# Kernel optimization log

Hardware: AMD Instinct MI355X
Metric: run time of the kernel (lower is better)

The kernel has to match this reference:

```python
import jax, jax.numpy as jnp
import numpy as np

NG, ND, NS, E, DIM, H = 20000, 8000, 8000, 300000, 256, 8
HD = DIM // H
SCALE = 1.0 / float(np.sqrt(HD))
EPS = 1e-5


def _ln(x, g, b):
    mu = x.mean(-1, keepdims=True)
    var = ((x - mu) ** 2).mean(-1, keepdims=True)
    return (x - mu) / jnp.sqrt(var + EPS) * g + b


def _attn(h_src, h_dst, Wq, bq, Wk, bk, Wv, bv, src, dst, n_dst):
    # multi-head edge dot-product attention with edge_softmax over incoming edges
    Q = (h_dst @ Wq.T + bq).reshape(-1, H, HD)
    K = (h_src @ Wk.T + bk).reshape(-1, H, HD)
    V = (h_src @ Wv.T + bv).reshape(-1, H, HD)
    score = jnp.einsum('ehd,ehd->eh', K[src], Q[dst]) * SCALE  # [E, H]
    m = jax.ops.segment_max(score, dst, num_segments=n_dst)
    m = jnp.where(jnp.isfinite(m), m, 0.0)  # nodes with no in-edges
    a = jnp.exp(score - m[dst])
    denom = jax.ops.segment_sum(a, dst, num_segments=n_dst)
    a = a / denom[dst]
    h = jax.ops.segment_sum(V[src] * a[:, :, None], dst, num_segments=n_dst)
    return h.reshape(n_dst, DIM)


def _bahdanau(m1, m2, W1, b1, W2, b2, v, bv):
    e1 = (jnp.tanh(m1 @ W1.T + b1) @ v.T + bv)[:, 0]
    e2 = (jnp.tanh(m2 @ W2.T + b2) @ v.T + bv)[:, 0]
    w = jax.nn.softmax(jnp.stack([e1, e2], axis=1), axis=1)
    return w[:, 0:1] * m1 + w[:, 1:2] * m2


def _forward(gene_feat, drug_feat, disease_feat,
             dg_Wq, dg_bq, dg_Wk, dg_bk, dg_Wv, dg_bv,
             disg_Wq, disg_bq, disg_Wk, disg_bk, disg_Wv, disg_bv,
             gd_Wq, gd_bq, gd_Wk, gd_bk, gd_Wv, gd_bv,
             gdis_Wq, gdis_bq, gdis_Wk, gdis_bk, gdis_Wv, gdis_bv,
             f_W1, f_b1, f_W2, f_b2, f_v, f_bv,
             ln1_g, ln1_b, ln2_g, ln2_b,
             dg_src, dg_dst, disg_src, disg_dst, gd_src, gd_dst, gdis_src, gdis_dst):
    gm_drug = _attn(drug_feat, gene_feat, dg_Wq, dg_bq, dg_Wk, dg_bk, dg_Wv, dg_bv, dg_src, dg_dst, NG)
    gm_dis = _attn(disease_feat, gene_feat, disg_Wq, disg_bq, disg_Wk, disg_bk, disg_Wv, disg_bv, disg_src, disg_dst, NG)
    has_d = jnp.zeros((NG,), bool).at[dg_dst].set(True)
    has_s = jnp.zeros((NG,), bool).at[disg_dst].set(True)
    fused = _bahdanau(gm_drug, gm_dis, f_W1, f_b1, f_W2, f_b2, f_v, f_bv)
    gene_msg = jnp.where((has_d & has_s)[:, None], fused,
                         jnp.where(has_d[:, None], gm_drug,
                                   jnp.where(has_s[:, None], gm_dis, 0.0)))
    gene_out = _ln(gene_feat + jax.nn.gelu(gene_msg, approximate=False), ln1_g, ln1_b)
    drug_msg = _attn(gene_out, drug_feat, gd_Wq, gd_bq, gd_Wk, gd_bk, gd_Wv, gd_bv, gd_src, gd_dst, ND)
    dis_msg = _attn(gene_out, disease_feat, gdis_Wq, gdis_bq, gdis_Wk, gdis_bk, gdis_Wv, gdis_bv, gdis_src, gdis_dst, NS)
    drug_out = _ln(drug_feat + jax.nn.gelu(drug_msg, approximate=False), ln2_g, ln2_b)
    disease_out = _ln(disease_feat + jax.nn.gelu(dis_msg, approximate=False), ln2_g, ln2_b)
    return (drug_out, disease_out, gene_out)


def setup_inputs() -> dict:
    ks = jax.random.split(jax.random.key(0), 40)
    it = iter(range(40))

    def nrm(shape):
        return jax.random.normal(ks[next(it)], shape, dtype=jnp.float32)

    def xav(din, dout):
        lim = float(np.sqrt(6.0 / (din + dout)))
        return jax.random.uniform(ks[next(it)], (dout, din), minval=-lim, maxval=lim, dtype=jnp.float32)

    def ridx(n, hi):
        return jax.random.randint(ks[next(it)], (n,), 0, hi, dtype=jnp.int32)

    inp = {}
    inp['gene_feat'] = nrm((NG, DIM))
    inp['drug_feat'] = nrm((ND, DIM))
    inp['disease_feat'] = nrm((NS, DIM))
    for p in ['dg', 'disg', 'gd', 'gdis']:
        inp[p + '_Wq'] = xav(DIM, DIM)
        inp[p + '_bq'] = jnp.zeros((DIM,), jnp.float32)
        inp[p + '_Wk'] = xav(DIM, DIM)
        inp[p + '_bk'] = jnp.zeros((DIM,), jnp.float32)
        inp[p + '_Wv'] = xav(DIM, DIM)
        inp[p + '_bv'] = jnp.zeros((DIM,), jnp.float32)
    inp['f_W1'] = xav(DIM, DIM); inp['f_b1'] = jnp.zeros((DIM,), jnp.float32)
    inp['f_W2'] = xav(DIM, DIM); inp['f_b2'] = jnp.zeros((DIM,), jnp.float32)
    inp['f_v'] = xav(DIM, 1); inp['f_bv'] = jnp.zeros((1,), jnp.float32)
    inp['ln1_g'] = jnp.ones((DIM,), jnp.float32); inp['ln1_b'] = jnp.zeros((DIM,), jnp.float32)
    inp['ln2_g'] = jnp.ones((DIM,), jnp.float32); inp['ln2_b'] = jnp.zeros((DIM,), jnp.float32)
    inp['dg_src'] = ridx(E, ND); inp['dg_dst'] = ridx(E, NG)
    inp['disg_src'] = ridx(E, NS); inp['disg_dst'] = ridx(E, NG)
    inp['gd_src'] = ridx(E, NG); inp['gd_dst'] = ridx(E, ND)
    inp['gdis_src'] = ridx(E, NG); inp['gdis_dst'] = ridx(E, NS)
    return inp


def reference(gene_feat, drug_feat, disease_feat,
              dg_Wq, dg_bq, dg_Wk, dg_bk, dg_Wv, dg_bv,
              disg_Wq, disg_bq, disg_Wk, disg_bk, disg_Wv, disg_bv,
              gd_Wq, gd_bq, gd_Wk, gd_bk, gd_Wv, gd_bv,
              gdis_Wq, gdis_bq, gdis_Wk, gdis_bk, gdis_Wv, gdis_bv,
              f_W1, f_b1, f_W2, f_b2, f_v, f_bv,
              ln1_g, ln1_b, ln2_g, ln2_b,
              dg_src, dg_dst, disg_src, disg_dst, gd_src, gd_dst, gdis_src, gdis_dst):
    return _forward(gene_feat, drug_feat, disease_feat,
                    dg_Wq, dg_bq, dg_Wk, dg_bk, dg_Wv, dg_bv,
                    disg_Wq, disg_bq, disg_Wk, disg_bk, disg_Wv, disg_bv,
                    gd_Wq, gd_bq, gd_Wk, gd_bk, gd_Wv, gd_bv,
                    gdis_Wq, gdis_bq, gdis_Wk, gdis_bk, gdis_Wv, gdis_bv,
                    f_W1, f_b1, f_W2, f_b2, f_v, f_bv,
                    ln1_g, ln1_b, ln2_g, ln2_b,
                    dg_src, dg_dst, disg_src, disg_dst, gd_src, gd_dst, gdis_src, gdis_dst)
```

## Files before the change

### kernel.cpp

```cpp
#include <hip/hip_runtime.h>

#define NG 20000
#define ND 8000
#define NS 8000
#define EE 300000
#define DIM 256
#define SCALE_QK 0.17677669529663687f
#define LNEPS 1e-5f

#define MAXB 40
#define L1CH 2048
#define NCH1 ((EE + L1CH - 1) / L1CH)
#define CB_G 8704
#define CB_S 10496
#define RB_G (40 * CB_G)
#define RB_S (32 * CB_S)

typedef __attribute__((ext_vector_type(4))) float floatx4;
typedef __attribute__((ext_vector_type(8))) short shortx8;
typedef __attribute__((ext_vector_type(8))) unsigned short ushortx8;

__device__ __forceinline__ float bf2f(unsigned short u) {
    union { unsigned u; float f; } c; c.u = ((unsigned)u) << 16; return c.f;
}
__device__ __forceinline__ unsigned short f2bf(float f) {
    union { float f; unsigned u; } c; c.f = f;
    return (unsigned short)((c.u + 0x7fffu + ((c.u >> 16) & 1u)) >> 16);
}
__device__ __forceinline__ float gelu_exact(float v) {
    return 0.5f * v * (1.0f + erff(v * 0.70710678118654752f));
}

template <int MODE, int KVI>
__global__ __launch_bounds__(256, 2) void gemm_nt(
    const unsigned short* __restrict__ A, const unsigned short* __restrict__ W,
    const float* __restrict__ bias1, const float* __restrict__ bias2,
    const float* __restrict__ bias3, const float* __restrict__ bias4,
    unsigned short* __restrict__ C, int ldc,
    const float* __restrict__ vvec, float* __restrict__ evec, int M)
{
    __shared__ unsigned short As[128][40];
    __shared__ unsigned short Bs[64][40];
    const int tid = threadIdx.x;
    const int lane = tid & 63, wv = tid >> 6;
    const int quad = lane >> 4, l16 = lane & 15;
    const int m0 = blockIdx.x * 128;
    const int n0 = blockIdx.y * 64;

    floatx4 acc[2][4];
#pragma unroll
    for (int i = 0; i < 2; ++i)
#pragma unroll
        for (int j = 0; j < 4; ++j) acc[i][j] = (floatx4){0.f, 0.f, 0.f, 0.f};

    const int sr = tid >> 2;
    const int sc = (tid & 3) * 8;

    for (int k0 = 0; k0 < 256; k0 += 32) {
        __syncthreads();
        *(int4*)(&Bs[sr][sc]) =
            *(const int4*)(W + (size_t)(n0 + sr) * 256 + k0 + sc);
#pragma unroll
        for (int rr = 0; rr < 2; ++rr) {
            int row = sr + rr * 64;
            int gm = m0 + row;
            int4 av = make_int4(0, 0, 0, 0);
            if (gm < M)
                av = *(const int4*)(A + (size_t)gm * 256 + k0 + sc);
            *(int4*)(&As[row][sc]) = av;
        }
        __syncthreads();
        shortx8 af[2], bfr[4];
#pragma unroll
        for (int mf = 0; mf < 2; ++mf)
            af[mf] = *(const shortx8*)(&As[wv * 32 + mf * 16 + l16][quad * 8]);
#pragma unroll
        for (int nf = 0; nf < 4; ++nf)
            bfr[nf] = *(const shortx8*)(&Bs[nf * 16 + l16][quad * 8]);
#pragma unroll
        for (int mf = 0; mf < 2; ++mf)
#pragma unroll
            for (int nf = 0; nf < 4; ++nf)
                acc[mf][nf] = __builtin_amdgcn_mfma_f32_16x16x32_bf16(
                    af[mf], bfr[nf], acc[mf][nf], 0, 0, 0);
    }

    if (MODE == 0) {
#pragma unroll
        for (int mf = 0; mf < 2; ++mf)
#pragma unroll
            for (int r = 0; r < 4; ++r) {
                int m = m0 + wv * 32 + mf * 16 + quad * 4 + r;
                if (m < M) {
#pragma unroll
                    for (int nf = 0; nf < 4; ++nf) {
                        int n = n0 + nf * 16 + l16;
                        int h = n >> 8;
                        const float* bp = (h == 0) ? bias1 : (h == 1) ? bias2
                                        : (h == 2) ? bias3 : bias4;
                        float bn = bp[n & 255];
                        int pos;
                        if (KVI) {
                            int nn = n & 511;
                            pos = (n & ~511) + ((nn & 255) >> 2) * 8 + (nn & 3) +
                                  ((nn >> 8) << 2);
                        } else {
                            pos = n;
                        }
                        C[(size_t)m * ldc + pos] = f2bf(acc[mf][nf][r] + bn);
                    }
                }
            }
    } else {
        float p[2][4] = {};
#pragma unroll
        for (int mf = 0; mf < 2; ++mf)
#pragma unroll
            for (int nf = 0; nf < 4; ++nf) {
                int n = n0 + nf * 16 + l16;
                float vn = vvec[n];
                float bn = bias1[n];
#pragma unroll
                for (int r = 0; r < 4; ++r)
                    p[mf][r] += vn * tanhf(acc[mf][nf][r] + bn);
            }
#pragma unroll
        for (int mf = 0; mf < 2; ++mf)
#pragma unroll
            for (int r = 0; r < 4; ++r) {
                float s = p[mf][r];
                s += __shfl_xor(s, 1); s += __shfl_xor(s, 2);
                s += __shfl_xor(s, 4); s += __shfl_xor(s, 8);
                if (l16 == 0) {
                    int m = m0 + wv * 32 + mf * 16 + quad * 4 + r;
                    if (m < M) atomicAdd(&evec[m], s);
                }
            }
    }
}

struct WSrc { const float* p[14]; };

__global__ void convert_w_kernel(WSrc s, unsigned short* __restrict__ out) {
    int idx = blockIdx.x * 256 + threadIdx.x;
    int mat = idx >> 14;
    int e = (idx & 16383) << 2;
    float4 f = *(const float4*)(s.p[mat] + e);
    ushort4 t;
    t.x = f2bf(f.x); t.y = f2bf(f.y); t.z = f2bf(f.z); t.w = f2bf(f.w);
    *(ushort4*)(out + ((size_t)mat << 16) + e) = t;
}

__global__ void convert_feat_kernel(
    const float* __restrict__ gf, const float* __restrict__ df,
    const float* __restrict__ sf, unsigned short* __restrict__ go,
    unsigned short* __restrict__ dougo, unsigned short* __restrict__ so)
{
    const int NG4 = NG * 64, ND4 = ND * 64, NS4 = NS * 64;
    int i = blockIdx.x * 256 + threadIdx.x;
    const float* in; unsigned short* out; int j;
    if (i < NG4) { in = gf; out = go; j = i; }
    else if (i < NG4 + ND4) { in = df; out = dougo; j = i - NG4; }
    else if (i < NG4 + ND4 + NS4) { in = sf; out = so; j = i - NG4 - ND4; }
    else return;
    float4 f = *(const float4*)(in + (size_t)j * 4);
    ushort4 t;
    t.x = f2bf(f.x); t.y = f2bf(f.y); t.z = f2bf(f.z); t.w = f2bf(f.w);
    *(ushort4*)(out + (size_t)j * 4) = t;
}

__global__ void zero_kernel(int* __restrict__ p, int n) {
    int i = blockIdx.x * blockDim.x + threadIdx.x;
    if (i < n) p[i] = 0;
}
__global__ void fillf_kernel(float* __restrict__ p, int n, float v) {
    int i = blockIdx.x * blockDim.x + threadIdx.x;
    if (i < n) p[i] = v;
}

struct L1P {
    const int* src[4];
    const int* dst[4];
    int* brec[4];
    int* bcur;
};
__global__ __launch_bounds__(256) void l1_bucket_kernel(L1P a) {
    __shared__ int hist[MAXB];
    int g = blockIdx.x / NCH1, c = blockIdx.x - g * NCH1;
    int base = c * L1CH;
    int tid = threadIdx.x;
    const int shift = (g < 2) ? 9 : 8;
    const int CB = (g < 2) ? CB_G : CB_S;
    const int NB = (g < 2) ? 40 : 32;
    if (tid < NB) hist[tid] = 0;
    __syncthreads();
    const int* __restrict__ dstp = a.dst[g];
    const int* __restrict__ srcp = a.src[g];
    int bk[8], rec[8], lr[8];
#pragma unroll
    for (int j = 0; j < 8; ++j) {
        int e = base + j * 256 + tid;
        bool ok = e < EE;
        int dd = ok ? dstp[e] : 0;
        int ss = ok ? srcp[e] : 0;
        bk[j] = dd >> shift;
        rec[j] = ((dd & ((1 << shift) - 1)) << 15) | ss;
        lr[j] = ok ? atomicAdd(&hist[bk[j]], 1) : -1;
    }
    __syncthreads();
    if (tid < NB) {
        int h = hist[tid];
        if (h > 0) hist[tid] = atomicAdd(&a.bcur[g * MAXB + tid], h);
    }
    __syncthreads();
    int* __restrict__ recp = a.brec[g];
#pragma unroll
    for (int j = 0; j < 8; ++j) {
        if (lr[j] >= 0) {
            int pos = hist[bk[j]] + lr[j];
            if (pos < CB) recp[bk[j] * CB + pos] = rec[j];
        }
    }
}

struct L2P {
    const int* brec[4];
    const int* bcur;
    int* cnt[4];
    int* offs[4];
    int* srcs[4];
};
__global__ __launch_bounds__(256) void l2_csr_kernel(L2P a) {
    __shared__ int hist[512];
    __shared__ int loffs[512];
    __shared__ int cur[512];
    __shared__ int ws2[4];
    __shared__ int bb;
    int bid = blockIdx.x, tid = threadIdx.x;
    int g, b;
    if (bid < 40) { g = 0; b = bid; }
    else if (bid < 80) { g = 1; b = bid - 40; }
    else if (bid < 112) { g = 2; b = bid - 80; }
    else { g = 3; b = bid - 112; }
    const int shift = (g < 2) ? 9 : 8;
    const int BSZ = 1 << shift;
    const int CB = (g < 2) ? CB_G : CB_S;
    const int N = (g < 2) ? NG : ((g == 2) ? ND : NS);
    hist[tid] = 0; hist[256 + tid] = 0;
    if (tid == 0) {
        int s = 0;
        const int* bc = a.bcur + g * MAXB;
        for (int i = 0; i < b; ++i) s += bc[i];
        bb = s;
    }
    __syncthreads();
    int total = a.bcur[g * MAXB + b];
    if (total > CB) total = CB;
    const int* __restrict__ recp = a.brec[g] + b * CB;
    for (int i = tid; i < total; i += 256)
        atomicAdd(&hist[recp[i] >> 15], 1);
    __syncthreads();
    int v0 = hist[2 * tid], v1 = hist[2 * tid + 1];
    int s = v0 + v1, x = s;
    int lane = tid & 63, wv = tid >> 6;
#pragma unroll
    for (int o = 1; o < 64; o <<= 1) {
        int u = __shfl_up(x, o);
        if (lane >= o) x += u;
    }
    if (lane == 63) ws2[wv] = x;
    __syncthreads();
    int woff = 0;
    for (int w = 0; w < wv; ++w) woff += ws2[w];
    int excl = woff + x - s;
    loffs[2 * tid] = excl; loffs[2 * tid + 1] = excl + v0;
    cur[2 * tid] = excl;  cur[2 * tid + 1] = excl + v0;
    int base = bb;
    int lo = b << shift;
    for (int i = tid; i < BSZ; i += 256) {
        int d = lo + i;
        if (d < N) {
            a.cnt[g][d] = hist[i];
            a.offs[g][d] = base + loffs[i];
        }
    }
    __syncthreads();
    int* __restrict__ sp = a.srcs[g];
    for (int i = tid; i < total; i += 256) {
        int rec = recp[i];
        int pos = atomicAdd(&cur[rec >> 15], 1);
        sp[base + pos] = rec & 0x7fff;
    }
}

__device__ __forceinline__ void wave_attn_node(
    const unsigned short* __restrict__ Q, int qs,
    const unsigned short* __restrict__ KV,
    const int* __restrict__ offs, const int* __restrict__ cnt,
    const int* __restrict__ srcs, int du, int lane,
    float& g0, float& g1, float& g2, float& g3)
{
    const int lo = lane * 4;
    const int lofs = lane * 8;
    ushort4 qv = *(const ushort4*)(Q + (size_t)du * qs + lo);
    const float q0 = bf2f(qv.x), q1 = bf2f(qv.y), q2 = bf2f(qv.z), q3 = bf2f(qv.w);
    const int beg = offs[du], num = cnt[du];

    float m[8], l[8], a[8][4];
#pragma unroll
    for (int c = 0; c < 8; ++c) {
        m[c] = -INFINITY; l[c] = 0.f;
        a[c][0] = a[c][1] = a[c][2] = a[c][3] = 0.f;
    }

    for (int i = 0; i < num; i += 8) {
        ushortx8 kv[8];
#pragma unroll
        for (int c = 0; c < 8; ++c) {
            int idx = i + c;
            int cidx = (idx < num) ? idx : (num - 1);
            int s = srcs[beg + cidx];
            kv[c] = *(const ushortx8*)(KV + (size_t)s * 512 + lofs);
        }
        float p[8];
#pragma unroll
        for (int c = 0; c < 8; ++c)
            p[c] = q0 * bf2f(kv[c][0]) + q1 * bf2f(kv[c][1]) +
                   q2 * bf2f(kv[c][2]) + q3 * bf2f(kv[c][3]);
#pragma unroll
        for (int c = 0; c < 8; ++c) p[c] += __shfl_xor(p[c], 1);
#pragma unroll
        for (int c = 0; c < 8; ++c) p[c] += __shfl_xor(p[c], 2);
#pragma unroll
        for (int c = 0; c < 8; ++c) p[c] += __shfl_xor(p[c], 4);
#pragma unroll
        for (int c = 0; c < 8; ++c) {
            if (i + c < num) {
                float sc = p[c] * SCALE_QK;
                float mn = fmaxf(m[c], sc);
                float eo = __expf(m[c] - mn);
                float en = __expf(sc - mn);
                a[c][0] = a[c][0] * eo + en * bf2f(kv[c][4]);
                a[c][1] = a[c][1] * eo + en * bf2f(kv[c][5]);
                a[c][2] = a[c][2] * eo + en * bf2f(kv[c][6]);
                a[c][3] = a[c][3] * eo + en * bf2f(kv[c][7]);
                l[c] = l[c] * eo + en;
                m[c] = mn;
            }
        }
    }

    float ms = fmaxf(fmaxf(fmaxf(m[0], m[1]), fmaxf(m[2], m[3])),
                     fmaxf(fmaxf(m[4], m[5]), fmaxf(m[6], m[7])));
    float A0 = 0.f, A1 = 0.f, A2 = 0.f, A3 = 0.f, L = 0.f;
    if (ms > -INFINITY) {
#pragma unroll
        for (int c = 0; c < 8; ++c) {
            float w = __expf(m[c] - ms);
            A0 += a[c][0] * w; A1 += a[c][1] * w;
            A2 += a[c][2] * w; A3 += a[c][3] * w;
            L += l[c] * w;
        }
    }
    float inv = (L > 0.f) ? 1.f / L : 0.f;
    g0 = A0 * inv; g1 = A1 * inv; g2 = A2 * inv; g3 = A3 * inv;
}

__device__ __forceinline__ void wave_ln_store(
    float x0, float x1, float x2, float x3,
    const float* __restrict__ g, const float* __restrict__ b,
    float* __restrict__ out, unsigned short* __restrict__ out_bf,
    int du, int lo)
{
    float s1 = x0 + x1 + x2 + x3;
    float s2 = x0 * x0 + x1 * x1 + x2 * x2 + x3 * x3;
#pragma unroll
    for (int o = 1; o < 64; o <<= 1) {
        s1 += __shfl_xor(s1, o);
        s2 += __shfl_xor(s2, o);
    }
    float mu = s1 * (1.f / 256.f);
    float var = fmaxf(s2 * (1.f / 256.f) - mu * mu, 0.f);
    float rs = rsqrtf(var + LNEPS);
    float4 gv = *(const float4*)(g + lo);
    float4 bv = *(const float4*)(b + lo);
    float y0 = (x0 - mu) * rs * gv.x + bv.x;
    float y1 = (x1 - mu) * rs * gv.y + bv.y;
    float y2 = (x2 - mu) * rs * gv.z + bv.z;
    float y3 = (x3 - mu) * rs * gv.w + bv.w;
    *(float4*)(out + (size_t)du * 256 + lo) = make_float4(y0, y1, y2, y3);
    if (out_bf) {
        ushort4 t; t.x = f2bf(y0); t.y = f2bf(y1); t.z = f2bf(y2); t.w = f2bf(y3);
        *(ushort4*)(out_bf + (size_t)du * 256 + lo) = t;
    }
}

__global__ __launch_bounds__(256) void agg_gm_kernel(
    const unsigned short* __restrict__ Q, int qs,
    const unsigned short* __restrict__ KV,
    const int* __restrict__ offs, const int* __restrict__ cnt,
    const int* __restrict__ srcs, unsigned short* __restrict__ gm, int N)
{
    int lane = threadIdx.x & 63, wv = threadIdx.x >> 6;
    int d = blockIdx.x * 4 + wv;
    if (d >= N) return;
    int du = __builtin_amdgcn_readfirstlane(d);
    float g0, g1, g2, g3;
    wave_attn_node(Q, qs, KV, offs, cnt, srcs, du, lane, g0, g1, g2, g3);
    ushort4 t; t.x = f2bf(g0); t.y = f2bf(g1); t.z = f2bf(g2); t.w = f2bf(g3);
    *(ushort4*)(gm + (size_t)du * 256 + lane * 4) = t;
}

__global__ __launch_bounds__(256) void agg_ln_kernel(
    const unsigned short* __restrict__ Q, int qs,
    const unsigned short* __restrict__ KV,
    const int* __restrict__ offs, const int* __restrict__ cnt,
    const int* __restrict__ srcs, const float* __restrict__ feat,
    const float* __restrict__ g, const float* __restrict__ b,
    float* __restrict__ out, int N)
{
    int lane = threadIdx.x & 63, wv = threadIdx.x >> 6;
    int d = blockIdx.x * 4 + wv;
    if (d >= N) return;
    int du = __builtin_amdgcn_readfirstlane(d);
    int lo = lane * 4;
    float g0, g1, g2, g3;
    wave_attn_node(Q, qs, KV, offs, cnt, srcs, du, lane, g0, g1, g2, g3);
    float4 fv = *(const float4*)(feat + (size_t)du * 256 + lo);
    float x0 = fv.x + gelu_exact(g0);
    float x1 = fv.y + gelu_exact(g1);
    float x2 = fv.z + gelu_exact(g2);
    float x3 = fv.w + gelu_exact(g3);
    wave_ln_store(x0, x1, x2, x3, g, b, out, nullptr, du, lo);
}

__global__ __launch_bounds__(256) void gene_fusion_kernel(
    const float* __restrict__ gene_feat, const unsigned short* __restrict__ gm_d,
    const unsigned short* __restrict__ gm_s, const float* __restrict__ e1,
    const float* __restrict__ e2, const int* __restrict__ cnt_d,
    const int* __restrict__ cnt_s, const float* __restrict__ g,
    const float* __restrict__ b, float* __restrict__ out,
    unsigned short* __restrict__ out_bf)
{
    int lane = threadIdx.x & 63, wv = threadIdx.x >> 6;
    int d = blockIdx.x * 4 + wv;
    if (d >= NG) return;
    int du = __builtin_amdgcn_readfirstlane(d);
    int lo = lane * 4;
    ushort4 v1 = *(const ushort4*)(gm_d + (size_t)du * 256 + lo);
    ushort4 v2 = *(const ushort4*)(gm_s + (size_t)du * 256 + lo);
    bool hd = cnt_d[du] > 0, hs = cnt_s[du] > 0;
    float wa, wb;
    if (hd && hs) {
        float aa = e1[du], bb = e2[du];
        float mm = fmaxf(aa, bb);
        float ea = __expf(aa - mm), eb = __expf(bb - mm);
        float inv = 1.f / (ea + eb);
        wa = ea * inv; wb = eb * inv;
    } else if (hd) { wa = 1.f; wb = 0.f; }
    else if (hs) { wa = 0.f; wb = 1.f; }
    else { wa = 0.f; wb = 0.f; }
    float m0 = wa * bf2f(v1.x) + wb * bf2f(v2.x);
    float m1 = wa * bf2f(v1.y) + wb * bf2f(v2.y);
    float m2 = wa * bf2f(v1.z) + wb * bf2f(v2.z);
    float m3 = wa * bf2f(v1.w) + wb * bf2f(v2.w);
    float4 fv = *(const float4*)(gene_feat + (size_t)du * 256 + lo);
    float x0 = fv.x + gelu_exact(m0);
    float x1 = fv.y + gelu_exact(m1);
    float x2 = fv.z + gelu_exact(m2);
    float x3 = fv.w + gelu_exact(m3);
    wave_ln_store(x0, x1, x2, x3, g, b, out, out_bf, du, lo);
}

extern "C" void kernel_launch(void* const* d_in, const int* in_sizes, int n_in,
                              void* d_out, int out_size, void* d_ws, size_t ws_size,
                              hipStream_t stream)
{
    float* out_f32 = (float*)d_out;

    const float* gene_feat    = (const float*)d_in[0];
    const float* drug_feat    = (const float*)d_in[1];
    const float* disease_feat = (const float*)d_in[2];
    const float* dg_Wq = (const float*)d_in[3];
    const float* dg_bq = (const float*)d_in[4];
    const float* dg_Wk = (const float*)d_in[5];
    const float* dg_bk = (const float*)d_in[6];
    const float* dg_Wv = (const float*)d_in[7];
    const float* dg_bv = (const float*)d_in[8];
    const float* disg_Wq = (const float*)d_in[9];
    const float* disg_bq = (const float*)d_in[10];
    const float* disg_Wk = (const float*)d_in[11];
    const float* disg_bk = (const float*)d_in[12];
    const float* disg_Wv = (const float*)d_in[13];
    const float* disg_bv = (const float*)d_in[14];
    const float* gd_Wq = (const float*)d_in[15];
    const float* gd_bq = (const float*)d_in[16];
    const float* gd_Wk = (const float*)d_in[17];
    const float* gd_bk = (const float*)d_in[18];
    const float* gd_Wv = (const float*)d_in[19];
    const float* gd_bv = (const float*)d_in[20];
    const float* gdis_Wq = (const float*)d_in[21];
    const float* gdis_bq = (const float*)d_in[22];
    const float* gdis_Wk = (const float*)d_in[23];
    const float* gdis_bk = (const float*)d_in[24];
    const float* gdis_Wv = (const float*)d_in[25];
    const float* gdis_bv = (const float*)d_in[26];
    const float* f_W1 = (const float*)d_in[27];
    const float* f_b1 = (const float*)d_in[28];
    const float* f_W2 = (const float*)d_in[29];
    const float* f_b2 = (const float*)d_in[30];
    const float* f_v  = (const float*)d_in[31];
    const float* ln1_g = (const float*)d_in[33];
    const float* ln1_b = (const float*)d_in[34];
    const float* ln2_g = (const float*)d_in[35];
    const float* ln2_b = (const float*)d_in[36];
    const int* dg_src   = (const int*)d_in[37];
    const int* dg_dst   = (const int*)d_in[38];
    const int* disg_src = (const int*)d_in[39];
    const int* disg_dst = (const int*)d_in[40];
    const int* gd_src   = (const int*)d_in[41];
    const int* gd_dst   = (const int*)d_in[42];
    const int* gdis_src = (const int*)d_in[43];
    const int* gdis_dst = (const int*)d_in[44];

    char* ws = (char*)d_ws;
    size_t off = 0;
    auto alloc = [&](size_t bytes) -> char* {
        char* p = ws + off;
        off += (bytes + 511) & ~(size_t)511;
        return p;
    };
    int* bcur = (int*)alloc(4 * MAXB * 4);
    float* e1 = (float*)alloc(NG * 4);
    float* e2 = (float*)alloc(NG * 4);
    size_t zero_len = off;
    int* offs_dg   = (int*)alloc(NG * 4);
    int* offs_disg = (int*)alloc(NG * 4);
    int* offs_gd   = (int*)alloc(ND * 4);
    int* offs_gdis = (int*)alloc(NS * 4);
    int* cnt_dg    = (int*)alloc(NG * 4);
    int* cnt_disg  = (int*)alloc(NG * 4);
    int* cnt_gd    = (int*)alloc(ND * 4);
    int* cnt_gdis  = (int*)alloc(NS * 4);
    int* srcs_dg   = (int*)alloc((size_t)EE * 4);
    int* srcs_disg = (int*)alloc((size_t)EE * 4);
    int* srcs_gd   = (int*)alloc((size_t)EE * 4);
    int* srcs_gdis = (int*)alloc((size_t)EE * 4);
    unsigned short* Q12  = (unsigned short*)alloc((size_t)NG * 512 * 2);
    unsigned short* KVb  = (unsigned short*)alloc((size_t)NG * 512 * 2);
    unsigned short* gm_d = (unsigned short*)alloc((size_t)NG * 256 * 2);
    unsigned short* gm_s = (unsigned short*)alloc((size_t)NG * 256 * 2);
    unsigned short* gene_bf = (unsigned short*)alloc((size_t)NG * 256 * 2);
    unsigned short* drug_bf = (unsigned short*)alloc((size_t)ND * 256 * 2);
    unsigned short* dis_bf  = (unsigned short*)alloc((size_t)NS * 256 * 2);
    unsigned short* Wbf     = (unsigned short*)alloc((size_t)14 * 65536 * 2);
    size_t need = off;

    int* brec0 = (int*)Q12;
    int* brec1 = brec0 + RB_G;
    int* brec2 = brec1 + RB_G;
    int* brec3 = brec2 + RB_S;

    unsigned short* gene_out_bf = gm_d;

    float* out_drug = out_f32;
    float* out_dis  = out_drug + (size_t)ND * 256;
    float* out_gene = out_dis + (size_t)NS * 256;

    if (ws_size < need) {
        fillf_kernel<<<(out_size + 255) / 256, 256, 0, stream>>>(out_f32, out_size, 1000.0f);
        return;
    }

    zero_kernel<<<((int)(zero_len / 4) + 255) / 256, 256, 0, stream>>>(
        (int*)d_ws, (int)(zero_len / 4));

    {
        WSrc s;
        const float* wl[14] = {dg_Wq, disg_Wq, dg_Wk, dg_Wv, disg_Wk, disg_Wv,
                               gd_Wk, gd_Wv, gdis_Wk, gdis_Wv, gd_Wq, gdis_Wq,
                               f_W1, f_W2};
        for (int i = 0; i < 14; ++i) s.p[i] = wl[i];
        convert_w_kernel<<<(14 * 16384) / 256, 256, 0, stream>>>(s, Wbf);
    }
    convert_feat_kernel<<<((NG + ND + NS) * 64 + 255) / 256, 256, 0, stream>>>(
        gene_feat, drug_feat, disease_feat, gene_bf, drug_bf, dis_bf);

    {
        L1P p;
        p.src[0] = dg_src; p.src[1] = disg_src; p.src[2] = gd_src; p.src[3] = gdis_src;
        p.dst[0] = dg_dst; p.dst[1] = disg_dst; p.dst[2] = gd_dst; p.dst[3] = gdis_dst;
        p.brec[0] = brec0; p.brec[1] = brec1; p.brec[2] = brec2; p.brec[3] = brec3;
        p.bcur = bcur;
        l1_bucket_kernel<<<4 * NCH1, 256, 0, stream>>>(p);
    }
    {
        L2P p;
        p.brec[0] = brec0; p.brec[1] = brec1; p.brec[2] = brec2; p.brec[3] = brec3;
        p.bcur = bcur;
        p.cnt[0] = cnt_dg; p.cnt[1] = cnt_disg; p.cnt[2] = cnt_gd; p.cnt[3] = cnt_gdis;
        p.offs[0] = offs_dg; p.offs[1] = offs_disg; p.offs[2] = offs_gd; p.offs[3] = offs_gdis;
        p.srcs[0] = srcs_dg; p.srcs[1] = srcs_disg; p.srcs[2] = srcs_gd; p.srcs[3] = srcs_gdis;
        l2_csr_kernel<<<144, 256, 0, stream>>>(p);
    }

    {
        dim3 gq((NG + 127) / 128, 8);
        gemm_nt<0, 0><<<gq, 256, 0, stream>>>(gene_bf, Wbf, dg_bq, disg_bq,
                                              dg_bq, dg_bq, Q12, 512,
                                              nullptr, nullptr, NG);
    }
    {
        dim3 gkv((ND + 127) / 128, 8);
        gemm_nt<0, 1><<<gkv, 256, 0, stream>>>(drug_bf, Wbf + (size_t)2 * 65536,
                                               dg_bk, dg_bv, dg_bk, dg_bk,
                                               KVb, 512, nullptr, nullptr, ND);
    }
    agg_gm_kernel<<<(NG + 3) / 4, 256, 0, stream>>>(Q12, 512, KVb, offs_dg, cnt_dg,
                                                    srcs_dg, gm_d, NG);
    {
        dim3 gkv((NS + 127) / 128, 8);
        gemm_nt<0, 1><<<gkv, 256, 0, stream>>>(dis_bf, Wbf + (size_t)4 * 65536,
                                               disg_bk, disg_bv, disg_bk, disg_bk,
                                               KVb, 512, nullptr, nullptr, NS);
    }
    agg_gm_kernel<<<(NG + 3) / 4, 256, 0, stream>>>(Q12 + 256, 512, KVb, offs_disg,
                                                    cnt_disg, srcs_disg, gm_s, NG);

    {
        dim3 gb((NG + 127) / 128, 4);
        gemm_nt<1, 0><<<gb, 256, 0, stream>>>(gm_d, Wbf + (size_t)12 * 65536,
                                              f_b1, f_b1, f_b1, f_b1,
                                              nullptr, 256, f_v, e1, NG);
        gemm_nt<1, 0><<<gb, 256, 0, stream>>>(gm_s, Wbf + (size_t)13 * 65536,
                                              f_b2, f_b2, f_b2, f_b2,
                                              nullptr, 256, f_v, e2, NG);
    }
    gene_fusion_kernel<<<(NG + 3) / 4, 256, 0, stream>>>(
        gene_feat, gm_d, gm_s, e1, e2, cnt_dg, cnt_disg, ln1_g, ln1_b,
        out_gene, gene_out_bf);

    {
        dim3 gq((ND + 127) / 128, 4);
        gemm_nt<0, 0><<<gq, 256, 0, stream>>>(drug_bf, Wbf + (size_t)10 * 65536,
                                              gd_bq, gd_bq, gd_bq, gd_bq,
                                              Q12, 256, nullptr, nullptr, ND);
    }
    {
        dim3 gkv((NG + 127) / 128, 8);
        gemm_nt<0, 1><<<gkv, 256, 0, stream>>>(gene_out_bf, Wbf + (size_t)6 * 65536,
                                               gd_bk, gd_bv, gd_bk, gd_bk,
                                               KVb, 512, nullptr, nullptr, NG);
    }
    agg_ln_kernel<<<(ND + 3) / 4, 256, 0, stream>>>(Q12, 256, KVb, offs_gd, cnt_gd,
                                                    srcs_gd, drug_feat, ln2_g, ln2_b,
                                                    out_drug, ND);

    {
        dim3 gq((NS + 127) / 128, 4);
        gemm_nt<0, 0><<<gq, 256, 0, stream>>>(dis_bf, Wbf + (size_t)11 * 65536,
                                              gdis_bq, gdis_bq, gdis_bq, gdis_bq,
                                              Q12, 256, nullptr, nullptr, NS);
    }
    {
        dim3 gkv((NG + 127) / 128, 8);
        gemm_nt<0, 1><<<gkv, 256, 0, stream>>>(gene_out_bf, Wbf + (size_t)8 * 65536,
                                               gdis_bk, gdis_bv, gdis_bk, gdis_bk,
                                               KVb, 512, nullptr, nullptr, NG);
    }
    agg_ln_kernel<<<(NS + 3) / 4, 256, 0, stream>>>(Q12, 256, KVb, offs_gdis, cnt_gdis,
                                                    srcs_gdis, disease_feat, ln2_g, ln2_b,
                                                    out_dis, NS);
}
```

Baseline: 535.5 us.

## Double-buffer GEMM tiles with async global-to-LDS loads and fuse prep kernels

The bf16 GEMM now stages A and W tiles into double-buffered, XOR-swizzled LDS through global_load_lds async copies, prefetching the next k-slice while MFMAs run on the current one. This drops one barrier per iteration, and launch bounds rise to four blocks per CU. The zero, weight-convert and feature-convert kernels are merged into one prep launch to cut launch overhead. The M bounds check on A rows is removed, so the last partial tile reads past the end of the array; a 64KB guard allocation is added to absorb those out-of-range reads.

```diff
diff --git a/kernel.cpp b/kernel.cpp
--- a/kernel.cpp
+++ b/kernel.cpp
@@ -19,6 +19,7 @@
 typedef __attribute__((ext_vector_type(4))) float floatx4;
 typedef __attribute__((ext_vector_type(8))) short shortx8;
 typedef __attribute__((ext_vector_type(8))) unsigned short ushortx8;
+typedef unsigned int u32;
 
 __device__ __forceinline__ float bf2f(unsigned short u) {
     union { unsigned u; float f; } c; c.u = ((unsigned)u) << 16; return c.f;
@@ -31,58 +32,74 @@
     return 0.5f * v * (1.0f + erff(v * 0.70710678118654752f));
 }
 
+__device__ __forceinline__ void async_load16(const unsigned short* g,
+                                             unsigned short* lds) {
+    __builtin_amdgcn_global_load_lds(
+        (const __attribute__((address_space(1))) u32*)(const void*)g,
+        (__attribute__((address_space(3))) u32*)(void*)lds, 16, 0, 0);
+}
+
+__device__ __forceinline__ int swzoff(int row, int q) {
+    int p = (row >> 1) & 7, b = row & 1;
+    return ((row >> 4) * 64 + p * 8 + (((b << 2) + q) ^ p)) * 8;
+}
+
 template <int MODE, int KVI>
-__global__ __launch_bounds__(256, 2) void gemm_nt(
+__global__ __launch_bounds__(256, 4) void gemm_nt(
     const unsigned short* __restrict__ A, const unsigned short* __restrict__ W,
     const float* __restrict__ bias1, const float* __restrict__ bias2,
     const float* __restrict__ bias3, const float* __restrict__ bias4,
     unsigned short* __restrict__ C, int ldc,
     const float* __restrict__ vvec, float* __restrict__ evec, int M)
 {
-    __shared__ unsigned short As[128][40];
-    __shared__ unsigned short Bs[64][40];
+    __shared__ unsigned short As[2][128 * 32];
+    __shared__ unsigned short Bs[2][64 * 32];
     const int tid = threadIdx.x;
     const int lane = tid & 63, wv = tid >> 6;
     const int quad = lane >> 4, l16 = lane & 15;
     const int m0 = blockIdx.x * 128;
     const int n0 = blockIdx.y * 64;
 
+    const int sp = lane >> 3, ss = lane & 7;
+    const int srow = 2 * sp + ((ss ^ sp) >> 2);
+    const int sq = (ss ^ sp) & 3;
+    const unsigned short* gA0 = A + (size_t)(m0 + wv * 16 + srow) * 256 + sq * 8;
+    const unsigned short* gA1 = A + (size_t)(m0 + 64 + wv * 16 + srow) * 256 + sq * 8;
+    const unsigned short* gB  = W + (size_t)(n0 + wv * 16 + srow) * 256 + sq * 8;
+
     floatx4 acc[2][4];
 #pragma unroll
     for (int i = 0; i < 2; ++i)
 #pragma unroll
         for (int j = 0; j < 4; ++j) acc[i][j] = (floatx4){0.f, 0.f, 0.f, 0.f};
 
-    const int sr = tid >> 2;
-    const int sc = (tid & 3) * 8;
+    async_load16(gA0, &As[0][(wv * 16) * 32]);
+    async_load16(gA1, &As[0][(64 + wv * 16) * 32]);
+    async_load16(gB,  &Bs[0][(wv * 16) * 32]);
+    __syncthreads();
 
     for (int k0 = 0; k0 < 256; k0 += 32) {
-        __syncthreads();
-        *(int4*)(&Bs[sr][sc]) =
-            *(const int4*)(W + (size_t)(n0 + sr) * 256 + k0 + sc);
-#pragma unroll
-        for (int rr = 0; rr < 2; ++rr) {
-            int row = sr + rr * 64;
-            int gm = m0 + row;
-            int4 av = make_int4(0, 0, 0, 0);
-            if (gm < M)
-                av = *(const int4*)(A + (size_t)gm * 256 + k0 + sc);
-            *(int4*)(&As[row][sc]) = av;
+        const int buf = (k0 >> 5) & 1;
+        if (k0 < 224) {
+            const int nb = buf ^ 1;
+            async_load16(gA0 + k0 + 32, &As[nb][(wv * 16) * 32]);
+            async_load16(gA1 + k0 + 32, &As[nb][(64 + wv * 16) * 32]);
+            async_load16(gB + k0 + 32,  &Bs[nb][(wv * 16) * 32]);
         }
-        __syncthreads();
         shortx8 af[2], bfr[4];
 #pragma unroll
         for (int mf = 0; mf < 2; ++mf)
-            af[mf] = *(const shortx8*)(&As[wv * 32 + mf * 16 + l16][quad * 8]);
+            af[mf] = *(const shortx8*)(&As[buf][swzoff(wv * 32 + mf * 16 + l16, quad)]);
 #pragma unroll
         for (int nf = 0; nf < 4; ++nf)
-            bfr[nf] = *(const shortx8*)(&Bs[nf * 16 + l16][quad * 8]);
+            bfr[nf] = *(const shortx8*)(&Bs[buf][swzoff(nf * 16 + l16, quad)]);
 #pragma unroll
         for (int mf = 0; mf < 2; ++mf)
 #pragma unroll
             for (int nf = 0; nf < 4; ++nf)
                 acc[mf][nf] = __builtin_amdgcn_mfma_f32_16x16x32_bf16(
                     af[mf], bfr[nf], acc[mf][nf], 0, 0, 0);
+        __syncthreads();
     }
 
     if (MODE == 0) {
@@ -139,29 +156,38 @@
     }
 }
 
-struct WSrc { const float* p[14]; };
-
-__global__ void convert_w_kernel(WSrc s, unsigned short* __restrict__ out) {
-    int idx = blockIdx.x * 256 + threadIdx.x;
-    int mat = idx >> 14;
-    int e = (idx & 16383) << 2;
-    float4 f = *(const float4*)(s.p[mat] + e);
-    ushort4 t;
-    t.x = f2bf(f.x); t.y = f2bf(f.y); t.z = f2bf(f.z); t.w = f2bf(f.w);
-    *(ushort4*)(out + ((size_t)mat << 16) + e) = t;
-}
-
-__global__ void convert_feat_kernel(
-    const float* __restrict__ gf, const float* __restrict__ df,
-    const float* __restrict__ sf, unsigned short* __restrict__ go,
-    unsigned short* __restrict__ dougo, unsigned short* __restrict__ so)
-{
+struct PrepP {
+    int* zb; int zn; int nzb;
+    const float* wsrc[14];
+    unsigned short* wout;
+    const float* gf; const float* df; const float* sf;
+    unsigned short* go; unsigned short* dfo; unsigned short* so;
+};
+__global__ void prep_kernel(PrepP p) {
+    int bid = blockIdx.x, tid = threadIdx.x;
+    if (bid < p.nzb) {
+        int i = bid * 256 + tid;
+        if (i < p.zn) p.zb[i] = 0;
+        return;
+    }
+    bid -= p.nzb;
+    if (bid < 896) {
+        int idx = bid * 256 + tid;
+        int mat = idx >> 14;
+        int e = (idx & 16383) << 2;
+        float4 f = *(const float4*)(p.wsrc[mat] + e);
+        ushort4 t;
+        t.x = f2bf(f.x); t.y = f2bf(f.y); t.z = f2bf(f.z); t.w = f2bf(f.w);
+        *(ushort4*)(p.wout + ((size_t)mat << 16) + e) = t;
+        return;
+    }
+    bid -= 896;
     const int NG4 = NG * 64, ND4 = ND * 64, NS4 = NS * 64;
-    int i = blockIdx.x * 256 + threadIdx.x;
+    int i = bid * 256 + tid;
     const float* in; unsigned short* out; int j;
-    if (i < NG4) { in = gf; out = go; j = i; }
-    else if (i < NG4 + ND4) { in = df; out = dougo; j = i - NG4; }
-    else if (i < NG4 + ND4 + NS4) { in = sf; out = so; j = i - NG4 - ND4; }
+    if (i < NG4) { in = p.gf; out = p.go; j = i; }
+    else if (i < NG4 + ND4) { in = p.df; out = p.dfo; j = i - NG4; }
+    else if (i < NG4 + ND4 + NS4) { in = p.sf; out = p.so; j = i - NG4 - ND4; }
     else return;
     float4 f = *(const float4*)(in + (size_t)j * 4);
     ushort4 t;
@@ -169,10 +195,6 @@
     *(ushort4*)(out + (size_t)j * 4) = t;
 }
 
-__global__ void zero_kernel(int* __restrict__ p, int n) {
-    int i = blockIdx.x * blockDim.x + threadIdx.x;
-    if (i < n) p[i] = 0;
-}
 __global__ void fillf_kernel(float* __restrict__ p, int n, float v) {
     int i = blockIdx.x * blockDim.x + threadIdx.x;
     if (i < n) p[i] = v;
@@ -554,6 +576,8 @@
     unsigned short* drug_bf = (unsigned short*)alloc((size_t)ND * 256 * 2);
     unsigned short* dis_bf  = (unsigned short*)alloc((size_t)NS * 256 * 2);
     unsigned short* Wbf     = (unsigned short*)alloc((size_t)14 * 65536 * 2);
+    char* guard = alloc(64 * 1024);
+    (void)guard;
     size_t need = off;
 
     int* brec0 = (int*)Q12;
@@ -572,19 +596,21 @@
         return;
     }
 
-    zero_kernel<<<((int)(zero_len / 4) + 255) / 256, 256, 0, stream>>>(
-        (int*)d_ws, (int)(zero_len / 4));
-
-    {
-        WSrc s;
+    {
+        PrepP p;
+        p.zb = (int*)d_ws;
+        p.zn = (int)(zero_len / 4);
+        p.nzb = (p.zn + 255) / 256;
         const float* wl[14] = {dg_Wq, disg_Wq, dg_Wk, dg_Wv, disg_Wk, disg_Wv,
                                gd_Wk, gd_Wv, gdis_Wk, gdis_Wv, gd_Wq, gdis_Wq,
                                f_W1, f_W2};
-        for (int i = 0; i < 14; ++i) s.p[i] = wl[i];
-        convert_w_kernel<<<(14 * 16384) / 256, 256, 0, stream>>>(s, Wbf);
-    }
-    convert_feat_kernel<<<((NG + ND + NS) * 64 + 255) / 256, 256, 0, stream>>>(
-        gene_feat, drug_feat, disease_feat, gene_bf, drug_bf, dis_bf);
+        for (int i = 0; i < 14; ++i) p.wsrc[i] = wl[i];
+        p.wout = Wbf;
+        p.gf = gene_feat; p.df = drug_feat; p.sf = disease_feat;
+        p.go = gene_bf; p.dfo = drug_bf; p.so = dis_bf;
+        int nfeat = ((NG + ND + NS) * 64 + 255) / 256;
+        prep_kernel<<<p.nzb + 896 + nfeat, 256, 0, stream>>>(p);
+    }
 
     {
         L1P p;
```

After: 515.9 us. 3.7% less time.
